# Optimization experiments

Measured on AMD Instinct MI355X. Metric: run time of the kernel, lower is better.

## Reference

```python
import jax, jax.numpy as jnp
import numpy as np
import math

L, C, NH = 6, 512, 8
HD = C // NH
FF = 4 * C
B = 16
IH, IW = 16, 64
RH, RW = 16, 16
T = IH * IW + RH * RW  # 1280 tokens


def _ln(x, w, b):
    m = jnp.mean(x, axis=-1, keepdims=True)
    v = jnp.mean((x - m) ** 2, axis=-1, keepdims=True)
    return (x - m) * jax.lax.rsqrt(v + 1e-5) * w + b


def setup_inputs() -> dict:
    key = jax.random.key(0)
    ks = jax.random.split(key, 16)
    s = 0.02  # gpt_linear_layer_init_std
    def w(k, shape):
        return jax.random.normal(k, shape, jnp.float32) * s
    return {
        "image_tensor": jax.random.normal(ks[0], (B, C, IH, IW), jnp.float32),
        "radar_tensor": jax.random.normal(ks[1], (B, C, RH, RW), jnp.float32),
        "pos_emb": w(ks[2], (1, T, C)),
        "ln1_w": jnp.ones((L, C), jnp.float32),
        "ln1_b": jnp.zeros((L, C), jnp.float32),
        "Wq": w(ks[3], (L, C, C)), "bq": jnp.zeros((L, C), jnp.float32),
        "Wk": w(ks[4], (L, C, C)), "bk": jnp.zeros((L, C), jnp.float32),
        "Wv": w(ks[5], (L, C, C)), "bv": jnp.zeros((L, C), jnp.float32),
        "Wo": w(ks[6], (L, C, C)), "bo": jnp.zeros((L, C), jnp.float32),
        "ln2_w": jnp.ones((L, C), jnp.float32),
        "ln2_b": jnp.zeros((L, C), jnp.float32),
        "W1": w(ks[7], (L, C, FF)), "b1": jnp.zeros((L, FF), jnp.float32),
        "W2": w(ks[8], (L, FF, C)), "b2": jnp.zeros((L, C), jnp.float32),
        "lnf_w": jnp.ones((C,), jnp.float32),
        "lnf_b": jnp.zeros((C,), jnp.float32),
    }


def reference(image_tensor, radar_tensor, pos_emb, ln1_w, ln1_b, Wq, bq, Wk, bk,
              Wv, bv, Wo, bo, ln2_w, ln2_b, W1, b1, W2, b2, lnf_w, lnf_b):
    bz = radar_tensor.shape[0]
    # (B,C,H,W) -> (B,H*W,C) tokens, channels become embedding dim
    img = jnp.transpose(image_tensor, (0, 2, 3, 1)).reshape(bz, IH * IW, C)
    rad = jnp.transpose(radar_tensor, (0, 2, 3, 1)).reshape(bz, RH * RW, C)
    x = pos_emb + jnp.concatenate([img, rad], axis=1)  # (B,T,C); dropout p=0
    scale = 1.0 / math.sqrt(HD)
    for i in range(L):
        h = _ln(x, ln1_w[i], ln1_b[i])
        q = (h @ Wq[i] + bq[i]).reshape(bz, T, NH, HD).transpose(0, 2, 1, 3)
        k = (h @ Wk[i] + bk[i]).reshape(bz, T, NH, HD).transpose(0, 2, 1, 3)
        v = (h @ Wv[i] + bv[i]).reshape(bz, T, NH, HD).transpose(0, 2, 1, 3)
        att = jax.nn.softmax(jnp.einsum('bhqd,bhkd->bhqk', q, k) * scale, axis=-1)
        y = jnp.einsum('bhqk,bhkd->bhqd', att, v)
        y = y.transpose(0, 2, 1, 3).reshape(bz, T, C)
        x = x + (y @ Wo[i] + bo[i])
        h2 = _ln(x, ln2_w[i], ln2_b[i])
        x = x + (jax.nn.relu(h2 @ W1[i] + b1[i]) @ W2[i] + b2[i])
    x = _ln(x, lnf_w, lnf_b)
    # torch .view reinterpretation of contiguous (B,T,C) memory as (B,C,h,w)
    img_out = x[:, :IH * IW, :].reshape(bz, C, IH, IW)
    rad_out = x[:, IH * IW:, :].reshape(bz, C, RH, RW)
    return (img_out, rad_out)
```

## Files before the change

### kernel.cpp

```cpp
#include <hip/hip_runtime.h>
#include <stdint.h>

typedef __attribute__((ext_vector_type(8))) short bf16x8;
typedef __attribute__((ext_vector_type(4))) short bf16x4;
typedef __attribute__((ext_vector_type(4))) float fx4;
typedef __attribute__((ext_vector_type(4))) unsigned short ushx4;
typedef unsigned short ush;

#define DEV __device__ __forceinline__

DEV unsigned short f2bf(float f) {
  unsigned u = __float_as_uint(f);
  u += 0x7fffu + ((u >> 16) & 1u);
  return (unsigned short)(u >> 16);
}

DEV float fast_exp2(float x) { return __builtin_amdgcn_exp2f(x); }

DEV unsigned pk_bf16(float a, float b) {
  unsigned r;
  asm("v_cvt_pk_bf16_f32 %0, %1, %2" : "=v"(r) : "v"(a), "v"(b));
  return r;
}

DEV void async16(const void* g, void* l) {
  __builtin_amdgcn_global_load_lds(
      (const __attribute__((address_space(1))) unsigned*)g,
      (__attribute__((address_space(3))) unsigned*)l, 16, 0, 0);
}

#define QSCALE 0.18033688011112042f

#define WSTRIDE 3145728

__global__ __launch_bounds__(256) void k_prep_weights(
    const float* __restrict__ Wq, const float* __restrict__ Wk,
    const float* __restrict__ Wv, const float* __restrict__ Wo,
    const float* __restrict__ W1, const float* __restrict__ W2,
    ush* __restrict__ wbf) {
  __shared__ float tile[32][33];
  int bid = blockIdx.x;
  int l = bid / 3072, r = bid % 3072;
  const float* src; ush* dst; int R, Cc, t;
  if (r < 768) {
    int w = r >> 8; t = r & 255; R = 512; Cc = 512;
    src = (w == 0 ? Wq : (w == 1 ? Wk : Wv)) + (size_t)l * 262144;
    dst = wbf + (size_t)l * WSTRIDE + w * 262144;
  } else if (r < 1024) {
    t = r - 768; R = 512; Cc = 512;
    src = Wo + (size_t)l * 262144; dst = wbf + (size_t)l * WSTRIDE + 786432;
  } else if (r < 2048) {
    t = r - 1024; R = 512; Cc = 2048;
    src = W1 + (size_t)l * 1048576; dst = wbf + (size_t)l * WSTRIDE + 1048576;
  } else {
    t = r - 2048; R = 2048; Cc = 512;
    src = W2 + (size_t)l * 1048576; dst = wbf + (size_t)l * WSTRIDE + 2097152;
  }
  int tpr = Cc >> 5;
  int trow = t / tpr, tcol = t % tpr;
  int tx = threadIdx.x & 31, ty = threadIdx.x >> 5;
#pragma unroll
  for (int i = 0; i < 4; i++) {
    int rr = trow * 32 + ty + i * 8, cc = tcol * 32 + tx;
    tile[ty + i * 8][tx] = src[(size_t)rr * Cc + cc];
  }
  __syncthreads();
#pragma unroll
  for (int i = 0; i < 4; i++) {
    int cc = tcol * 32 + ty + i * 8, rr = trow * 32 + tx;
    dst[(size_t)cc * R + rr] = f2bf(tile[tx][ty + i * 8]);
  }
}

__global__ __launch_bounds__(256) void k_pack_bias(
    const float* __restrict__ bq, const float* __restrict__ bk,
    const float* __restrict__ bv, float* __restrict__ dst) {
  int idx = blockIdx.x * 256 + threadIdx.x;
  if (idx >= 6 * 1536) return;
  int l = idx / 1536, r = idx % 1536;
  float v = (r < 512) ? bq[l * 512 + r]
            : (r < 1024) ? bk[l * 512 + r - 512] : bv[l * 512 + r - 1024];
  dst[idx] = v;
}

__global__ __launch_bounds__(256) void k_embed(
    const float* __restrict__ img, const float* __restrict__ rad,
    const float* __restrict__ pos, float* __restrict__ x) {
  __shared__ float tile[32][33];
  int bid = blockIdx.x;
  int b = bid / 640, r2 = bid % 640;
  int tc = r2 / 40, tt = r2 % 40;
  int tx = threadIdx.x & 31, ty = threadIdx.x >> 5;
#pragma unroll
  for (int i = 0; i < 4; i++) {
    int c = tc * 32 + ty + i * 8, t = tt * 32 + tx;
    float v = (t < 1024) ? img[(size_t)(b * 512 + c) * 1024 + t]
                         : rad[(size_t)(b * 512 + c) * 256 + (t - 1024)];
    tile[ty + i * 8][tx] = v;
  }
  __syncthreads();
#pragma unroll
  for (int i = 0; i < 4; i++) {
    int t = tt * 32 + ty + i * 8, c = tc * 32 + tx;
    x[(size_t)(b * 1280 + t) * 512 + c] = tile[tx][ty + i * 8] + pos[(size_t)t * 512 + c];
  }
}

__global__ __launch_bounds__(256) void k_ln_bf16(
    const float* __restrict__ x, const float* __restrict__ w,
    const float* __restrict__ bia, ush* __restrict__ h) {
  int wave = threadIdx.x >> 6, lane = threadIdx.x & 63;
  int row = blockIdx.x * 4 + wave;
  int c0 = lane * 8;
  const float4* xr = (const float4*)(x + (size_t)row * 512 + c0);
  float4 a = xr[0], b4 = xr[1];
  float v[8] = {a.x, a.y, a.z, a.w, b4.x, b4.y, b4.z, b4.w};
  float s = 0.f, s2 = 0.f;
#pragma unroll
  for (int e = 0; e < 8; e++) { s += v[e]; s2 += v[e] * v[e]; }
#pragma unroll
  for (int mask = 1; mask < 64; mask <<= 1) {
    s += __shfl_xor(s, mask, 64);
    s2 += __shfl_xor(s2, mask, 64);
  }
  float mean = s * (1.f / 512.f);
  float var = s2 * (1.f / 512.f) - mean * mean;
  float rstd = rsqrtf(var + 1e-5f);
  bf16x8 o;
#pragma unroll
  for (int e = 0; e < 8; e++)
    o[e] = (short)f2bf((v[e] - mean) * rstd * w[c0 + e] + bia[c0 + e]);
  *(bf16x8*)(h + (size_t)row * 512 + c0) = o;
}

__global__ __launch_bounds__(256) void k_ln_final(
    const float* __restrict__ x, const float* __restrict__ w,
    const float* __restrict__ bia, float* __restrict__ out) {
  int wave = threadIdx.x >> 6, lane = threadIdx.x & 63;
  int row = blockIdx.x * 4 + wave;
  int c0 = lane * 8;
  const float4* xr = (const float4*)(x + (size_t)row * 512 + c0);
  float4 a = xr[0], b4 = xr[1];
  float v[8] = {a.x, a.y, a.z, a.w, b4.x, b4.y, b4.z, b4.w};
  float s = 0.f, s2 = 0.f;
#pragma unroll
  for (int e = 0; e < 8; e++) { s += v[e]; s2 += v[e] * v[e]; }
#pragma unroll
  for (int mask = 1; mask < 64; mask <<= 1) {
    s += __shfl_xor(s, mask, 64);
    s2 += __shfl_xor(s2, mask, 64);
  }
  float mean = s * (1.f / 512.f);
  float var = s2 * (1.f / 512.f) - mean * mean;
  float rstd = rsqrtf(var + 1e-5f);
  int b = row / 1280, t = row % 1280;
  size_t orow = (t < 1024) ? ((size_t)b * 1024 + t)
                           : (16384 + (size_t)b * 256 + (t - 1024));
  float o[8];
#pragma unroll
  for (int e = 0; e < 8; e++)
    o[e] = (v[e] - mean) * rstd * w[c0 + e] + bia[c0 + e];
  float4* op = (float4*)(out + orow * 512 + c0);
  op[0] = make_float4(o[0], o[1], o[2], o[3]);
  op[1] = make_float4(o[4], o[5], o[6], o[7]);
}

template <int MODE>
__global__ __launch_bounds__(256) void k_gemm(
    const ush* __restrict__ A, const ush* __restrict__ Wt,
    const float* __restrict__ bias, void* __restrict__ outv,
    ush* __restrict__ vt2, int M, int N, int K) {
  __shared__ char smem[32768];
  char* As = smem;
  char* Bs = smem + 16384;
  const int tid = threadIdx.x;
  const int m0 = blockIdx.y << 7, n0 = blockIdx.x << 7;
  const int lane = tid & 63, wave = tid >> 6;
  const int quad = lane >> 4, l16 = lane & 15;
  const int m_off = (wave & 1) << 6, n_off = (wave >> 1) << 6;
  fx4 acc[4][4];
#pragma unroll
  for (int a = 0; a < 4; a++)
#pragma unroll
    for (int b = 0; b < 4; b++) acc[a][b] = (fx4){0.f, 0.f, 0.f, 0.f};

  for (int k0 = 0; k0 < K; k0 += 64) {
#pragma unroll
    for (int j = 0; j < 4; j++) {
      int f = (j << 8) + tid;
      int row = f >> 3, cph = f & 7;
      int clog = cph ^ (row & 7);
      async16(A + (size_t)(m0 + row) * K + k0 + (clog << 3), As + (f << 4));
    }
#pragma unroll
    for (int j = 0; j < 4; j++) {
      int f = (j << 8) + tid;
      int row = f >> 3, cph = f & 7;
      int clog = cph ^ (row & 7);
      async16(Wt + (size_t)(n0 + row) * K + k0 + (clog << 3), Bs + (f << 4));
    }
    __syncthreads();
#pragma unroll
    for (int ks = 0; ks < 2; ks++) {
      const int chunk = (ks << 2) + quad;
      bf16x8 af[4], bfr[4];
#pragma unroll
      for (int mb = 0; mb < 4; mb++) {
        int rw = m_off + (mb << 4) + l16;
        af[mb] = *(const bf16x8*)(As + rw * 128 + ((chunk ^ (rw & 7)) << 4));
      }
#pragma unroll
      for (int nb = 0; nb < 4; nb++) {
        int rw = n_off + (nb << 4) + l16;
        bfr[nb] = *(const bf16x8*)(Bs + rw * 128 + ((chunk ^ (rw & 7)) << 4));
      }
#pragma unroll
      for (int mb = 0; mb < 4; mb++)
#pragma unroll
        for (int nb = 0; nb < 4; nb++)
          acc[mb][nb] = __builtin_amdgcn_mfma_f32_16x16x32_bf16(
              af[mb], bfr[nb], acc[mb][nb], 0, 0, 0);
    }
    __syncthreads();
  }
#pragma unroll
  for (int mb = 0; mb < 4; mb++) {
#pragma unroll
    for (int nb = 0; nb < 4; nb++) {
      int col = n0 + n_off + (nb << 4) + l16;
      float bval = bias[col];
      if (MODE == 3 && col >= 1024) {
        int row0 = m0 + m_off + (mb << 4) + (quad << 2);
        int b = row0 / 1280, t = row0 - b * 1280;
        int u0 = t & 31;
        int p0 = ((u0 >> 2) & 3) * 8 + ((u0 & 16) >> 2);
        int tp = (t & ~31) + p0;
        ushx4 pk;
#pragma unroll
        for (int i = 0; i < 4; i++) pk[i] = f2bf(acc[mb][nb][i] + bval);
        *(ushx4*)(vt2 + ((size_t)(b * 512 + col - 1024)) * 1280 + tp) = pk;
      } else {
#pragma unroll
        for (int i = 0; i < 4; i++) {
          int row = m0 + m_off + (mb << 4) + (quad << 2) + i;
          float v = acc[mb][nb][i] + bval;
          if (MODE == 1) v = fmaxf(v, 0.f);
          if (MODE == 0 || MODE == 1) {
            ((ush*)outv)[(size_t)row * N + col] = f2bf(v);
          } else if (MODE == 3) {
            if (col < 512) v *= QSCALE;
            ((ush*)outv)[(size_t)row * 1024 + col] = f2bf(v);
          } else {
            float* X = (float*)outv;
            X[(size_t)row * N + col] += v;
          }
        }
      }
    }
  }
}

__global__ __launch_bounds__(256) void k_attn(const ush* __restrict__ qk,
                                              const ush* __restrict__ vt,
                                              ush* __restrict__ y) {
  __shared__ char smem[16384];
  char* Ks = smem;
  char* Vs = smem + 8192;
  int id = blockIdx.x;
  int xcd = id & 7, slot = id >> 3;
  int bh = xcd * 16 + slot / 20;
  int qt = slot % 20;
  int b = bh >> 3, h = bh & 7;
  int tid = threadIdx.x;
  int lane = tid & 63, wave = tid >> 6;
  int quad = lane >> 4, l16 = lane & 15;
  int qbase = qt * 64 + wave * 16;

  const ush* qp = qk + (size_t)(b * 1280 + qbase + l16) * 1024 + h * 64 + quad * 8;
  bf16x8 bq0 = *(const bf16x8*)qp;
  bf16x8 bq1 = *(const bf16x8*)(qp + 32);

  const ush* kbase = qk + (size_t)(b * 1280) * 1024 + 512 + h * 64;
  const ush* vbase = vt + (size_t)(b * 512 + h * 64) * 1280;

  bf16x8 ones;
#pragma unroll
  for (int e = 0; e < 8; e++) ones[e] = (short)0x3F80;

  fx4 yacc[4];
#pragma unroll
  for (int nb = 0; nb < 4; nb++) yacc[nb] = (fx4){0.f, 0.f, 0.f, 0.f};
  fx4 ysum = (fx4){0.f, 0.f, 0.f, 0.f};

  for (int k0 = 0; k0 < 1280; k0 += 64) {
#pragma unroll
    for (int j = 0; j < 2; j++) {
      int f = (j << 8) + tid;
      int key = f >> 3, cph = f & 7, clog = cph ^ (key & 7);
      async16(kbase + (size_t)(k0 + key) * 1024 + (clog << 3), Ks + (f << 4));
    }
#pragma unroll
    for (int j = 0; j < 2; j++) {
      int f = (j << 8) + tid;
      int d = f >> 3, cph = f & 7, clog = cph ^ (d & 7);
      async16(vbase + (size_t)d * 1280 + k0 + (clog << 3), Vs + (f << 4));
    }
    __syncthreads();
#pragma unroll
    for (int g = 0; g < 2; g++) {
      int r0 = g * 32 + l16, r1 = g * 32 + 16 + l16;
      bf16x8 ka0 = *(const bf16x8*)(Ks + r0 * 128 + ((quad ^ (r0 & 7)) << 4));
      bf16x8 ka1 = *(const bf16x8*)(Ks + r0 * 128 + (((4 + quad) ^ (r0 & 7)) << 4));
      bf16x8 kc0 = *(const bf16x8*)(Ks + r1 * 128 + ((quad ^ (r1 & 7)) << 4));
      bf16x8 kc1 = *(const bf16x8*)(Ks + r1 * 128 + (((4 + quad) ^ (r1 & 7)) << 4));
      fx4 s0 = (fx4){0.f, 0.f, 0.f, 0.f}, s1 = (fx4){0.f, 0.f, 0.f, 0.f};
      s0 = __builtin_amdgcn_mfma_f32_16x16x32_bf16(ka0, bq0, s0, 0, 0, 0);
      s0 = __builtin_amdgcn_mfma_f32_16x16x32_bf16(ka1, bq1, s0, 0, 0, 0);
      s1 = __builtin_amdgcn_mfma_f32_16x16x32_bf16(kc0, bq0, s1, 0, 0, 0);
      s1 = __builtin_amdgcn_mfma_f32_16x16x32_bf16(kc1, bq1, s1, 0, 0, 0);
      float p0 = fast_exp2(s0[0]), p1 = fast_exp2(s0[1]);
      float p2 = fast_exp2(s0[2]), p3 = fast_exp2(s0[3]);
      float p4 = fast_exp2(s1[0]), p5 = fast_exp2(s1[1]);
      float p6 = fast_exp2(s1[2]), p7 = fast_exp2(s1[3]);
      unsigned w0 = pk_bf16(p0, p1), w1 = pk_bf16(p2, p3);
      unsigned w2 = pk_bf16(p4, p5), w3 = pk_bf16(p6, p7);
      int4 pi = make_int4((int)w0, (int)w1, (int)w2, (int)w3);
      bf16x8 pf = *(bf16x8*)&pi;
      ysum = __builtin_amdgcn_mfma_f32_16x16x32_bf16(pf, ones, ysum, 0, 0, 0);
#pragma unroll
      for (int nb = 0; nb < 4; nb++) {
        int d = nb * 16 + l16;
        bf16x8 vf = *(const bf16x8*)(Vs + d * 128 +
                                     (((g * 4 + quad) ^ (d & 7)) << 4));
        yacc[nb] = __builtin_amdgcn_mfma_f32_16x16x32_bf16(pf, vf, yacc[nb], 0, 0, 0);
      }
    }
    __syncthreads();
  }
  float rl[4];
#pragma unroll
  for (int i = 0; i < 4; i++) rl[i] = 1.0f / ysum[i];
#pragma unroll
  for (int nb = 0; nb < 4; nb++)
#pragma unroll
    for (int i = 0; i < 4; i++) {
      int t = qbase + quad * 4 + i;
      int col = h * 64 + nb * 16 + l16;
      y[(size_t)(b * 1280 + t) * 512 + col] = f2bf(yacc[nb][i] * rl[i]);
    }
}

extern "C" void kernel_launch(void* const* d_in, const int* in_sizes, int n_in,
                              void* d_out, int out_size, void* d_ws, size_t ws_size,
                              hipStream_t stream) {
  const float* img = (const float*)d_in[0];
  const float* rad = (const float*)d_in[1];
  const float* pos = (const float*)d_in[2];
  const float* ln1w = (const float*)d_in[3];
  const float* ln1b = (const float*)d_in[4];
  const float* Wq = (const float*)d_in[5];
  const float* bq = (const float*)d_in[6];
  const float* Wk = (const float*)d_in[7];
  const float* bk = (const float*)d_in[8];
  const float* Wv = (const float*)d_in[9];
  const float* bv = (const float*)d_in[10];
  const float* Wo = (const float*)d_in[11];
  const float* bo = (const float*)d_in[12];
  const float* ln2w = (const float*)d_in[13];
  const float* ln2b = (const float*)d_in[14];
  const float* W1 = (const float*)d_in[15];
  const float* b1 = (const float*)d_in[16];
  const float* W2 = (const float*)d_in[17];
  const float* b2 = (const float*)d_in[18];
  const float* lnfw = (const float*)d_in[19];
  const float* lnfb = (const float*)d_in[20];

  char* ws = (char*)d_ws;
  float* xw = (float*)(ws + 0);
  ush* h    = (ush*)(ws + 41943040);
  ush* qk   = (ush*)(ws + 62914560);
  ush* vt   = (ush*)(ws + 104857600);
  ush* y    = (ush*)(ws + 125829120);
  ush* u    = (ush*)(ws + 62914560);
  ush* wbf  = (ush*)(ws + 146800640);
  float* qkvb = (float*)(ws + 184549376);

  k_prep_weights<<<18432, 256, 0, stream>>>(Wq, Wk, Wv, Wo, W1, W2, wbf);
  k_pack_bias<<<36, 256, 0, stream>>>(bq, bk, bv, qkvb);
  k_embed<<<10240, 256, 0, stream>>>(img, rad, pos, xw);

  for (int l = 0; l < 6; l++) {
    const ush* wl = wbf + (size_t)l * WSTRIDE;
    k_ln_bf16<<<5120, 256, 0, stream>>>(xw, ln1w + l * 512, ln1b + l * 512, h);
    k_gemm<3><<<dim3(12, 160), 256, 0, stream>>>(h, wl, qkvb + l * 1536, qk, vt, 20480, 1536, 512);
    k_attn<<<2560, 256, 0, stream>>>(qk, vt, y);
    k_gemm<2><<<dim3(4, 160), 256, 0, stream>>>(y, wl + 786432, bo + l * 512, xw, nullptr, 20480, 512, 512);
    k_ln_bf16<<<5120, 256, 0, stream>>>(xw, ln2w + l * 512, ln2b + l * 512, h);
    k_gemm<1><<<dim3(16, 160), 256, 0, stream>>>(h, wl + 1048576, b1 + l * 2048, u, nullptr, 20480, 2048, 512);
    k_gemm<2><<<dim3(4, 160), 256, 0, stream>>>(u, wl + 2097152, b2 + l * 512, xw, nullptr, 20480, 512, 2048);
  }
  k_ln_final<<<5120, 256, 0, stream>>>(xw, lnfw, lnfb, (float*)d_out);
}
```

Measured before the change: 2.037 ms.

## Store residual stream in bf16 and swizzle GEMM blocks across XCDs

Converts the fp32 residual activation buffer to bf16, so embed, layernorm and the residual-add GEMM epilogue read and write half the bytes. It also remaps GEMM block indices so that each XCD processes a contiguous set of M strips, which is meant to improve L2 reuse of the A tiles. The trade-off is accumulated bf16 rounding error in the residual across all layers, which risks accuracy drift against the fp32 reference.

```diff
diff --git a/kernel.cpp b/kernel.cpp
--- a/kernel.cpp
+++ b/kernel.cpp
@@ -14,6 +14,8 @@
   u += 0x7fffu + ((u >> 16) & 1u);
   return (unsigned short)(u >> 16);
 }
+
+DEV float bf2f(ush u) { return __uint_as_float(((unsigned)u) << 16); }
 
 DEV float fast_exp2(float x) { return __builtin_amdgcn_exp2f(x); }
 
@@ -85,7 +87,7 @@
 
 __global__ __launch_bounds__(256) void k_embed(
     const float* __restrict__ img, const float* __restrict__ rad,
-    const float* __restrict__ pos, float* __restrict__ x) {
+    const float* __restrict__ pos, ush* __restrict__ x) {
   __shared__ float tile[32][33];
   int bid = blockIdx.x;
   int b = bid / 640, r2 = bid % 640;
@@ -102,19 +104,21 @@
 #pragma unroll
   for (int i = 0; i < 4; i++) {
     int t = tt * 32 + ty + i * 8, c = tc * 32 + tx;
-    x[(size_t)(b * 1280 + t) * 512 + c] = tile[tx][ty + i * 8] + pos[(size_t)t * 512 + c];
+    x[(size_t)(b * 1280 + t) * 512 + c] =
+        f2bf(tile[tx][ty + i * 8] + pos[(size_t)t * 512 + c]);
   }
 }
 
 __global__ __launch_bounds__(256) void k_ln_bf16(
-    const float* __restrict__ x, const float* __restrict__ w,
+    const ush* __restrict__ x, const float* __restrict__ w,
     const float* __restrict__ bia, ush* __restrict__ h) {
   int wave = threadIdx.x >> 6, lane = threadIdx.x & 63;
   int row = blockIdx.x * 4 + wave;
   int c0 = lane * 8;
-  const float4* xr = (const float4*)(x + (size_t)row * 512 + c0);
-  float4 a = xr[0], b4 = xr[1];
-  float v[8] = {a.x, a.y, a.z, a.w, b4.x, b4.y, b4.z, b4.w};
+  bf16x8 xi = *(const bf16x8*)(x + (size_t)row * 512 + c0);
+  float v[8];
+#pragma unroll
+  for (int e = 0; e < 8; e++) v[e] = bf2f((ush)xi[e]);
   float s = 0.f, s2 = 0.f;
 #pragma unroll
   for (int e = 0; e < 8; e++) { s += v[e]; s2 += v[e] * v[e]; }
@@ -134,14 +138,15 @@
 }
 
 __global__ __launch_bounds__(256) void k_ln_final(
-    const float* __restrict__ x, const float* __restrict__ w,
+    const ush* __restrict__ x, const float* __restrict__ w,
     const float* __restrict__ bia, float* __restrict__ out) {
   int wave = threadIdx.x >> 6, lane = threadIdx.x & 63;
   int row = blockIdx.x * 4 + wave;
   int c0 = lane * 8;
-  const float4* xr = (const float4*)(x + (size_t)row * 512 + c0);
-  float4 a = xr[0], b4 = xr[1];
-  float v[8] = {a.x, a.y, a.z, a.w, b4.x, b4.y, b4.z, b4.w};
+  bf16x8 xi = *(const bf16x8*)(x + (size_t)row * 512 + c0);
+  float v[8];
+#pragma unroll
+  for (int e = 0; e < 8; e++) v[e] = bf2f((ush)xi[e]);
   float s = 0.f, s2 = 0.f;
 #pragma unroll
   for (int e = 0; e < 8; e++) { s += v[e]; s2 += v[e] * v[e]; }
@@ -174,7 +179,13 @@
   char* As = smem;
   char* Bs = smem + 16384;
   const int tid = threadIdx.x;
-  const int m0 = blockIdx.y << 7, n0 = blockIdx.x << 7;
+  int id = blockIdx.y * gridDim.x + blockIdx.x;
+  int xcd = id & 7, s = id >> 3;
+  int nb_n = gridDim.x;
+  int strips_per_xcd = gridDim.y >> 3;
+  int mblk = xcd * strips_per_xcd + s / nb_n;
+  int nblk = s % nb_n;
+  const int m0 = mblk << 7, n0 = nblk << 7;
   const int lane = tid & 63, wave = tid >> 6;
   const int quad = lane >> 4, l16 = lane & 15;
   const int m_off = (wave & 1) << 6, n_off = (wave >> 1) << 6;
@@ -251,8 +262,9 @@
             if (col < 512) v *= QSCALE;
             ((ush*)outv)[(size_t)row * 1024 + col] = f2bf(v);
           } else {
-            float* X = (float*)outv;
-            X[(size_t)row * N + col] += v;
+            ush* X = (ush*)outv;
+            size_t idx = (size_t)row * N + col;
+            X[idx] = f2bf(bf2f(X[idx]) + v);
           }
         }
       }
@@ -376,7 +388,7 @@
   const float* lnfb = (const float*)d_in[20];
 
   char* ws = (char*)d_ws;
-  float* xw = (float*)(ws + 0);
+  ush* xw   = (ush*)(ws + 0);
   ush* h    = (ush*)(ws + 41943040);
   ush* qk   = (ush*)(ws + 62914560);
   ush* vt   = (ush*)(ws + 104857600);
```

New measurement: 2.041 ms. No clear change (+0.2%).

## Double attention query tile per wave and remap GEMM blocks per XCD

Applied to the files above, without the earlier changes.

The attention kernel now handles two 16-row query tiles per wave (128 queries per block). Each K/V tile loaded into LDS is reused across twice as many MFMAs, and the grid is halved. The GEMM kernels remap block IDs so that each XCD works on a contiguous set of M strips, which is meant to improve L2 locality for shared A rows. In exchange the attention kernel uses more registers and launches fewer blocks, and the GEMM remap assumes gridDim.y is divisible by 8.

```diff
diff --git a/kernel.cpp b/kernel.cpp
--- a/kernel.cpp
+++ b/kernel.cpp
@@ -14,6 +14,8 @@
   u += 0x7fffu + ((u >> 16) & 1u);
   return (unsigned short)(u >> 16);
 }
+
+DEV float bf2f(ush u) { return __uint_as_float(((unsigned)u) << 16); }
 
 DEV float fast_exp2(float x) { return __builtin_amdgcn_exp2f(x); }
 
@@ -174,7 +176,13 @@
   char* As = smem;
   char* Bs = smem + 16384;
   const int tid = threadIdx.x;
-  const int m0 = blockIdx.y << 7, n0 = blockIdx.x << 7;
+  int id = blockIdx.y * gridDim.x + blockIdx.x;
+  int xcd = id & 7, s = id >> 3;
+  int nb_n = gridDim.x;
+  int strips_per_xcd = gridDim.y >> 3;
+  int mblk = xcd * strips_per_xcd + s / nb_n;
+  int nblk = s % nb_n;
+  const int m0 = mblk << 7, n0 = nblk << 7;
   const int lane = tid & 63, wave = tid >> 6;
   const int quad = lane >> 4, l16 = lane & 15;
   const int m_off = (wave & 1) << 6, n_off = (wave >> 1) << 6;
@@ -268,17 +276,20 @@
   char* Vs = smem + 8192;
   int id = blockIdx.x;
   int xcd = id & 7, slot = id >> 3;
-  int bh = xcd * 16 + slot / 20;
-  int qt = slot % 20;
+  int bh = xcd * 16 + slot / 10;
+  int qt = slot % 10;
   int b = bh >> 3, h = bh & 7;
   int tid = threadIdx.x;
   int lane = tid & 63, wave = tid >> 6;
   int quad = lane >> 4, l16 = lane & 15;
-  int qbase = qt * 64 + wave * 16;
-
-  const ush* qp = qk + (size_t)(b * 1280 + qbase + l16) * 1024 + h * 64 + quad * 8;
-  bf16x8 bq0 = *(const bf16x8*)qp;
-  bf16x8 bq1 = *(const bf16x8*)(qp + 32);
+  int qbase = qt * 128 + wave * 32;
+
+  const ush* qp0 = qk + (size_t)(b * 1280 + qbase + l16) * 1024 + h * 64 + quad * 8;
+  const ush* qp1 = qp0 + (size_t)16 * 1024;
+  bf16x8 bq0 = *(const bf16x8*)qp0;
+  bf16x8 bq1 = *(const bf16x8*)(qp0 + 32);
+  bf16x8 bq2 = *(const bf16x8*)qp1;
+  bf16x8 bq3 = *(const bf16x8*)(qp1 + 32);
 
   const ush* kbase = qk + (size_t)(b * 1280) * 1024 + 512 + h * 64;
   const ush* vbase = vt + (size_t)(b * 512 + h * 64) * 1280;
@@ -287,10 +298,14 @@
 #pragma unroll
   for (int e = 0; e < 8; e++) ones[e] = (short)0x3F80;
 
-  fx4 yacc[4];
-#pragma unroll
-  for (int nb = 0; nb < 4; nb++) yacc[nb] = (fx4){0.f, 0.f, 0.f, 0.f};
-  fx4 ysum = (fx4){0.f, 0.f, 0.f, 0.f};
+  fx4 yacc[2][4];
+#pragma unroll
+  for (int t = 0; t < 2; t++)
+#pragma unroll
+    for (int nb = 0; nb < 4; nb++) yacc[t][nb] = (fx4){0.f, 0.f, 0.f, 0.f};
+  fx4 ysum[2];
+  ysum[0] = (fx4){0.f, 0.f, 0.f, 0.f};
+  ysum[1] = (fx4){0.f, 0.f, 0.f, 0.f};
 
   for (int k0 = 0; k0 < 1280; k0 += 64) {
 #pragma unroll
@@ -313,41 +328,62 @@
       bf16x8 ka1 = *(const bf16x8*)(Ks + r0 * 128 + (((4 + quad) ^ (r0 & 7)) << 4));
       bf16x8 kc0 = *(const bf16x8*)(Ks + r1 * 128 + ((quad ^ (r1 & 7)) << 4));
       bf16x8 kc1 = *(const bf16x8*)(Ks + r1 * 128 + (((4 + quad) ^ (r1 & 7)) << 4));
-      fx4 s0 = (fx4){0.f, 0.f, 0.f, 0.f}, s1 = (fx4){0.f, 0.f, 0.f, 0.f};
-      s0 = __builtin_amdgcn_mfma_f32_16x16x32_bf16(ka0, bq0, s0, 0, 0, 0);
-      s0 = __builtin_amdgcn_mfma_f32_16x16x32_bf16(ka1, bq1, s0, 0, 0, 0);
-      s1 = __builtin_amdgcn_mfma_f32_16x16x32_bf16(kc0, bq0, s1, 0, 0, 0);
-      s1 = __builtin_amdgcn_mfma_f32_16x16x32_bf16(kc1, bq1, s1, 0, 0, 0);
-      float p0 = fast_exp2(s0[0]), p1 = fast_exp2(s0[1]);
-      float p2 = fast_exp2(s0[2]), p3 = fast_exp2(s0[3]);
-      float p4 = fast_exp2(s1[0]), p5 = fast_exp2(s1[1]);
-      float p6 = fast_exp2(s1[2]), p7 = fast_exp2(s1[3]);
-      unsigned w0 = pk_bf16(p0, p1), w1 = pk_bf16(p2, p3);
-      unsigned w2 = pk_bf16(p4, p5), w3 = pk_bf16(p6, p7);
-      int4 pi = make_int4((int)w0, (int)w1, (int)w2, (int)w3);
-      bf16x8 pf = *(bf16x8*)&pi;
-      ysum = __builtin_amdgcn_mfma_f32_16x16x32_bf16(pf, ones, ysum, 0, 0, 0);
+      fx4 s00 = (fx4){0.f, 0.f, 0.f, 0.f}, s10 = (fx4){0.f, 0.f, 0.f, 0.f};
+      fx4 s01 = (fx4){0.f, 0.f, 0.f, 0.f}, s11 = (fx4){0.f, 0.f, 0.f, 0.f};
+      s00 = __builtin_amdgcn_mfma_f32_16x16x32_bf16(ka0, bq0, s00, 0, 0, 0);
+      s00 = __builtin_amdgcn_mfma_f32_16x16x32_bf16(ka1, bq1, s00, 0, 0, 0);
+      s10 = __builtin_amdgcn_mfma_f32_16x16x32_bf16(kc0, bq0, s10, 0, 0, 0);
+      s10 = __builtin_amdgcn_mfma_f32_16x16x32_bf16(kc1, bq1, s10, 0, 0, 0);
+      s01 = __builtin_amdgcn_mfma_f32_16x16x32_bf16(ka0, bq2, s01, 0, 0, 0);
+      s01 = __builtin_amdgcn_mfma_f32_16x16x32_bf16(ka1, bq3, s01, 0, 0, 0);
+      s11 = __builtin_amdgcn_mfma_f32_16x16x32_bf16(kc0, bq2, s11, 0, 0, 0);
+      s11 = __builtin_amdgcn_mfma_f32_16x16x32_bf16(kc1, bq3, s11, 0, 0, 0);
+      bf16x8 pf0, pf1;
+      {
+        float p0 = fast_exp2(s00[0]), p1 = fast_exp2(s00[1]);
+        float p2 = fast_exp2(s00[2]), p3 = fast_exp2(s00[3]);
+        float p4 = fast_exp2(s10[0]), p5 = fast_exp2(s10[1]);
+        float p6 = fast_exp2(s10[2]), p7 = fast_exp2(s10[3]);
+        int4 pi = make_int4((int)pk_bf16(p0, p1), (int)pk_bf16(p2, p3),
+                            (int)pk_bf16(p4, p5), (int)pk_bf16(p6, p7));
+        pf0 = *(bf16x8*)&pi;
+      }
+      {
+        float p0 = fast_exp2(s01[0]), p1 = fast_exp2(s01[1]);
+        float p2 = fast_exp2(s01[2]), p3 = fast_exp2(s01[3]);
+        float p4 = fast_exp2(s11[0]), p5 = fast_exp2(s11[1]);
+        float p6 = fast_exp2(s11[2]), p7 = fast_exp2(s11[3]);
+        int4 pi = make_int4((int)pk_bf16(p0, p1), (int)pk_bf16(p2, p3),
+                            (int)pk_bf16(p4, p5), (int)pk_bf16(p6, p7));
+        pf1 = *(bf16x8*)&pi;
+      }
+      ysum[0] = __builtin_amdgcn_mfma_f32_16x16x32_bf16(pf0, ones, ysum[0], 0, 0, 0);
+      ysum[1] = __builtin_amdgcn_mfma_f32_16x16x32_bf16(pf1, ones, ysum[1], 0, 0, 0);
 #pragma unroll
       for (int nb = 0; nb < 4; nb++) {
         int d = nb * 16 + l16;
         bf16x8 vf = *(const bf16x8*)(Vs + d * 128 +
                                      (((g * 4 + quad) ^ (d & 7)) << 4));
-        yacc[nb] = __builtin_amdgcn_mfma_f32_16x16x32_bf16(pf, vf, yacc[nb], 0, 0, 0);
+        yacc[0][nb] = __builtin_amdgcn_mfma_f32_16x16x32_bf16(pf0, vf, yacc[0][nb], 0, 0, 0);
+        yacc[1][nb] = __builtin_amdgcn_mfma_f32_16x16x32_bf16(pf1, vf, yacc[1][nb], 0, 0, 0);
       }
     }
     __syncthreads();
   }
-  float rl[4];
-#pragma unroll
-  for (int i = 0; i < 4; i++) rl[i] = 1.0f / ysum[i];
-#pragma unroll
-  for (int nb = 0; nb < 4; nb++)
-#pragma unroll
-    for (int i = 0; i < 4; i++) {
-      int t = qbase + quad * 4 + i;
-      int col = h * 64 + nb * 16 + l16;
-      y[(size_t)(b * 1280 + t) * 512 + col] = f2bf(yacc[nb][i] * rl[i]);
-    }
+#pragma unroll
+  for (int t = 0; t < 2; t++) {
+    float rl[4];
+#pragma unroll
+    for (int i = 0; i < 4; i++) rl[i] = 1.0f / ysum[t][i];
+#pragma unroll
+    for (int nb = 0; nb < 4; nb++)
+#pragma unroll
+      for (int i = 0; i < 4; i++) {
+        int tr = qbase + t * 16 + quad * 4 + i;
+        int col = h * 64 + nb * 16 + l16;
+        y[(size_t)(b * 1280 + tr) * 512 + col] = f2bf(yacc[t][nb][i] * rl[i]);
+      }
+  }
 }
 
 extern "C" void kernel_launch(void* const* d_in, const int* in_sizes, int n_in,
@@ -393,7 +429,7 @@
     const ush* wl = wbf + (size_t)l * WSTRIDE;
     k_ln_bf16<<<5120, 256, 0, stream>>>(xw, ln1w + l * 512, ln1b + l * 512, h);
     k_gemm<3><<<dim3(12, 160), 256, 0, stream>>>(h, wl, qkvb + l * 1536, qk, vt, 20480, 1536, 512);
-    k_attn<<<2560, 256, 0, stream>>>(qk, vt, y);
+    k_attn<<<1280, 256, 0, stream>>>(qk, vt, y);
     k_gemm<2><<<dim3(4, 160), 256, 0, stream>>>(y, wl + 786432, bo + l * 512, xw, nullptr, 20480, 512, 512);
     k_ln_bf16<<<5120, 256, 0, stream>>>(xw, ln2w + l * 512, ln2b + l * 512, h);
     k_gemm<1><<<dim3(16, 160), 256, 0, stream>>>(h, wl + 1048576, b1 + l * 2048, u, nullptr, 20480, 2048, 512);
```

After: 1.955 ms. 1.04x faster.
